# Kernel optimization log

Hardware: AMD Instinct MI355X
Metric: run time of the kernel (lower is better)

## Reference

```python
import jax, jax.numpy as jnp
import numpy as np

B = 4; E_PER = 100_000; E = B * E_PER
N_NODES = 50_000; N_REL = 500; D = 64; D_LG = 256
K_PER_VI = 20; S_VI = E // K_PER_VI          # 20000 sorted vi segments
S_VJ_PER = 5_000; S_VJ = B * S_VJ_PER        # 20000 unsorted vj segments
N_MEM = 131_072
INTERACT = ((0, 3), (0, 2, 3), (0, 4), (0, 2, 4), (1, 3), (1, 2, 3), (1, 4), (1, 2, 4))


def _build_edges():
    rng = np.random.default_rng(0)
    idx_vi = np.repeat(np.arange(S_VI), K_PER_VI)          # sorted segment ids
    gpb = S_VI // B
    eg = idx_vi // gpb                                     # sorted by eg_idx too
    vi = rng.integers(0, N_NODES, S_VI)[idx_vi]
    idx_vj = np.empty(E, dtype=np.int64)
    for b in range(B):
        loc = np.concatenate([np.arange(S_VJ_PER), rng.integers(0, S_VJ_PER, E_PER - S_VJ_PER)])
        rng.shuffle(loc)
        idx_vj[b * E_PER:(b + 1) * E_PER] = b * S_VJ_PER + loc  # every group non-empty
    vj = rng.integers(0, N_NODES, S_VJ)[idx_vj]            # consistent (eg, vj) per group
    rel = rng.integers(0, N_REL, E)
    e2vi = rng.integers(0, N_MEM, E)
    e2vj = rng.integers(0, N_MEM, E)
    return np.stack([eg, vi, vj, rel, idx_vi, idx_vj, e2vi, e2vj], axis=1).astype(np.int32)


def setup_inputs() -> dict:
    key = jax.random.key(0)
    ks = jax.random.split(key, 10)
    return {
        "node_attention": jax.random.uniform(ks[0], (B, N_NODES), jnp.float32),
        "scanned_edges": jnp.asarray(_build_edges()),
        "edges_y": jax.random.uniform(ks[1], (E,), jnp.float32),
        "hidden_uncon": jax.random.normal(ks[2], (1, N_NODES, D_LG), jnp.float32),
        "hidden_con": jax.random.normal(ks[3], (N_MEM, D), jnp.float32),
        "Wc": jax.random.normal(ks[4], (D, D), jnp.float32) / np.sqrt(D).astype(np.float32),
        "bc": jnp.zeros((D,), jnp.float32),
        "Wu": jax.random.normal(ks[5], (D_LG, D), jnp.float32) / np.sqrt(D_LG).astype(np.float32),
        "bu": jnp.zeros((D,), jnp.float32),
        "rel_table": jax.random.normal(ks[6], (N_REL, D), jnp.float32) * 0.05,
        "ws": jax.random.normal(ks[7], (len(INTERACT), D), jnp.float32) / np.sqrt(float(len(INTERACT))).astype(np.float32) if False else jax.random.normal(ks[7], (len(INTERACT), D), jnp.float32) * (1.0 / np.sqrt(len(INTERACT)).astype(np.float32)),
        "fb": jnp.zeros((D,), jnp.float32),
        "out_w": jax.random.normal(ks[8], (D,), jnp.float32),
        "out_b": jnp.zeros((D,), jnp.float32),
        "n_vi_segments": S_VI,
        "n_vj_segments": S_VJ,
    }


def reference(node_attention, scanned_edges, edges_y, hidden_uncon, hidden_con,
              Wc, bc, Wu, bu, rel_table, ws, fb, out_w, out_b,
              n_vi_segments, n_vj_segments):
    eg, vi, vj, rel = (scanned_edges[:, i] for i in range(4))
    idx_vi, idx_vj, e2vi, e2vj = (scanned_edges[:, i] for i in range(4, 8))
    # projections (proj_con / proj_uncon, tanh Dense)
    hc = jnp.tanh(hidden_con @ Wc + bc)          # [N_MEM, D]
    hu = jnp.tanh(hidden_uncon @ Wu + bu)[0]     # [n_nodes, D]; batch_size==1 path of Node2Edge
    # Node2Edge gathers
    feats = (hc[e2vi], hu[vi], rel_table[rel], hc[e2vj], hu[vj])  # each [E, D]
    # F layer: weighted sum of elementwise interaction products
    out = fb
    for k, idxs in enumerate(INTERACT):
        x = feats[idxs[0]]
        for i in idxs[1:]:
            x = x * feats[i]
        out = out + x * ws[k]
    out = jax.nn.relu(out) * out_w + out_b
    logits = jnp.sum(out, axis=1)                # [E]
    # NeighborSoftmax at 'vi' (sorted segment softmax)
    m = jax.ops.segment_max(logits, idx_vi, num_segments=n_vi_segments)
    ex = jnp.exp(logits - m[idx_vi])
    den = jax.ops.segment_sum(ex, idx_vi, num_segments=n_vi_segments)
    transition = ex / den[idx_vi]
    # attention flow: gather source attention, weight, aggregate at vj
    trans_att = transition * node_attention[eg, vi] * edges_y
    aggr = jax.ops.segment_sum(trans_att, idx_vj, num_segments=n_vj_segments)
    b_g = jax.ops.segment_max(eg, idx_vj, num_segments=n_vj_segments)
    vj_g = jax.ops.segment_max(vj, idx_vj, num_segments=n_vj_segments)
    new_node_attention = jnp.zeros_like(node_attention).at[b_g, vj_g].add(aggr)
    return new_node_attention
```

## Files before the change

kernel.cpp:

```cpp
#include <hip/hip_runtime.h>
#include <hip/hip_bf16.h>
#include <type_traits>

#define D 64
#define KPER 20

typedef __attribute__((ext_vector_type(8))) short short8;
typedef __attribute__((ext_vector_type(4))) float floatx4;

__device__ __forceinline__ unsigned short f2bfu(float x) {
    __hip_bfloat16 h = __float2bfloat16(x);
    return *reinterpret_cast<unsigned short*>(&h);
}
__device__ __forceinline__ float bfu2f(unsigned short u) {
    return __uint_as_float(((unsigned)u) << 16);
}

__device__ __forceinline__ float fast_tanh(float x) {
    float xc = fminf(fmaxf(x, -15.f), 15.f);
    float e = __expf(2.f * xc);
    return 1.f - 2.f * __builtin_amdgcn_rcpf(1.f + e);
}

template<int CTRL>
__device__ __forceinline__ float dpp_add(float x) {
    int t = __builtin_amdgcn_update_dpp(0, __float_as_int(x), CTRL, 0xf, 0xf, true);
    return x + __int_as_float(t);
}
template<int CTRL>
__device__ __forceinline__ float dpp_max(float x) {
    int xi = __float_as_int(x);
    int t = __builtin_amdgcn_update_dpp(xi, xi, CTRL, 0xf, 0xf, false);
    return fmaxf(x, __int_as_float(t));
}
__device__ __forceinline__ float wave_sum_b(float x) {
    x = dpp_add<0x111>(x); x = dpp_add<0x112>(x);
    x = dpp_add<0x114>(x); x = dpp_add<0x118>(x);
    x = dpp_add<0x142>(x); x = dpp_add<0x143>(x);
    return __int_as_float(__builtin_amdgcn_readlane(__float_as_int(x), 63));
}
__device__ __forceinline__ float wave_max_b(float x) {
    x = dpp_max<0x111>(x); x = dpp_max<0x112>(x);
    x = dpp_max<0x114>(x); x = dpp_max<0x118>(x);
    x = dpp_max<0x142>(x); x = dpp_max<0x143>(x);
    return __int_as_float(__builtin_amdgcn_readlane(__float_as_int(x), 63));
}
__device__ __forceinline__ float row16_sum(float x) {
    x = dpp_add<0x111>(x); x = dpp_add<0x112>(x);
    x = dpp_add<0x114>(x); x = dpp_add<0x118>(x);
    return x;
}

__global__ __launch_bounds__(256) void prep(
        const float* __restrict__ Wc, const float* __restrict__ Wu,
        const float* __restrict__ relf,
        unsigned short* __restrict__ Wcp, unsigned short* __restrict__ Wup,
        unsigned short* __restrict__ relb, float* __restrict__ outz,
        int nout, int nrel) {
    int tid = blockIdx.x * 256 + threadIdx.x;
    int nth = gridDim.x * 256;
    for (int i = tid; i < 4 * 2 * 64 * 8; i += nth) {
        int j = i & 7, lane = (i >> 3) & 63, f = i >> 9;
        int ct = f >> 1, kt = f & 1;
        int m = lane & 15, quad = lane >> 4;
        Wcp[i] = f2bfu(Wc[(kt * 32 + quad * 8 + j) * 64 + ct * 16 + m]);
    }
    for (int i = tid; i < 4 * 8 * 64 * 8; i += nth) {
        int j = i & 7, lane = (i >> 3) & 63, f = i >> 9;
        int ct = f >> 3, kt = f & 7;
        int m = lane & 15, quad = lane >> 4;
        Wup[i] = f2bfu(Wu[(kt * 32 + quad * 8 + j) * 64 + ct * 16 + m]);
    }
    for (int i = tid; i < nrel; i += nth) relb[i] = f2bfu(relf[i]);
    for (int i = tid; i < nout; i += nth) outz[i] = 0.0f;
}

__device__ __forceinline__ void proj64_pair(const float* __restrict__ h,
        const unsigned short* __restrict__ Wp, const float* __restrict__ b,
        unsigned short* __restrict__ out, int rt0) {
    constexpr int K = 64, KT = 2, CTN = 4;
    int lane = threadIdx.x & 63;
    int m = lane & 15, quad = lane >> 4;
    short8 bfr[CTN][KT];
    #pragma unroll
    for (int ct = 0; ct < CTN; ++ct)
        #pragma unroll
        for (int kt = 0; kt < KT; ++kt)
            bfr[ct][kt] = *(const short8*)(Wp + (((ct * 2 + kt) * 64 + lane) << 3));
    float bv[CTN];
    #pragma unroll
    for (int ct = 0; ct < CTN; ++ct) bv[ct] = b[ct * 16 + m];
    int rt1 = rt0 + 1;
    const float* hrow0 = h + (size_t)(rt0 * 16 + m) * K + quad * 8;
    const float* hrow1 = h + (size_t)(rt1 * 16 + m) * K + quad * 8;
    floatx4 a0[KT][2], a1[KT][2];
    #pragma unroll
    for (int kt = 0; kt < KT; ++kt) {
        a0[kt][0] = *(const floatx4*)(hrow0 + kt * 32);
        a0[kt][1] = *(const floatx4*)(hrow0 + kt * 32 + 4);
        a1[kt][0] = *(const floatx4*)(hrow1 + kt * 32);
        a1[kt][1] = *(const floatx4*)(hrow1 + kt * 32 + 4);
    }
    #pragma unroll
    for (int t = 0; t < 2; ++t) {
        floatx4 (*ar)[2] = t ? a1 : a0;
        int rt = t ? rt1 : rt0;
        floatx4 acc[CTN];
        #pragma unroll
        for (int ct = 0; ct < CTN; ++ct) acc[ct] = floatx4{0.f, 0.f, 0.f, 0.f};
        #pragma unroll
        for (int kt = 0; kt < KT; ++kt) {
            short8 af;
            #pragma unroll
            for (int j = 0; j < 4; ++j) {
                af[j]     = (short)f2bfu(ar[kt][0][j]);
                af[j + 4] = (short)f2bfu(ar[kt][1][j]);
            }
            #pragma unroll
            for (int ct = 0; ct < CTN; ++ct)
                acc[ct] = __builtin_amdgcn_mfma_f32_16x16x32_bf16(af, bfr[ct][kt], acc[ct], 0, 0, 0);
        }
        #pragma unroll
        for (int ct = 0; ct < CTN; ++ct) {
            int col = ct * 16 + m;
            #pragma unroll
            for (int reg = 0; reg < 4; ++reg) {
                int row = rt * 16 + quad * 4 + reg;
                out[(size_t)row * 64 + col] = f2bfu(fast_tanh(acc[ct][reg] + bv[ct]));
            }
        }
    }
}

__device__ __forceinline__ void proj256_body(const float* __restrict__ h,
        const unsigned short* __restrict__ Wp, const float* __restrict__ b,
        unsigned short* __restrict__ out, int ct0, int rt0, int rtstride, int ntiles) {
    constexpr int K = 256, KT = 8, CTN = 2;
    int lane = threadIdx.x & 63;
    int m = lane & 15, quad = lane >> 4;
    short8 bfr[CTN][KT];
    #pragma unroll
    for (int ct = 0; ct < CTN; ++ct)
        #pragma unroll
        for (int kt = 0; kt < KT; ++kt)
            bfr[ct][kt] = *(const short8*)(Wp + ((((ct0 + ct) * 8 + kt) * 64 + lane) << 3));
    float bv[CTN];
    #pragma unroll
    for (int ct = 0; ct < CTN; ++ct) bv[ct] = b[(ct0 + ct) * 16 + m];
    for (int rt = rt0; rt < ntiles; rt += rtstride) {
        floatx4 acc[CTN];
        #pragma unroll
        for (int ct = 0; ct < CTN; ++ct) acc[ct] = floatx4{0.f, 0.f, 0.f, 0.f};
        const float* hrow = h + (size_t)(rt * 16 + m) * K + quad * 8;
        #pragma unroll
        for (int kt = 0; kt < KT; ++kt) {
            floatx4 v0 = *(const floatx4*)(hrow + kt * 32);
            floatx4 v1 = *(const floatx4*)(hrow + kt * 32 + 4);
            short8 af;
            #pragma unroll
            for (int j = 0; j < 4; ++j) {
                af[j]     = (short)f2bfu(v0[j]);
                af[j + 4] = (short)f2bfu(v1[j]);
            }
            #pragma unroll
            for (int ct = 0; ct < CTN; ++ct)
                acc[ct] = __builtin_amdgcn_mfma_f32_16x16x32_bf16(af, bfr[ct][kt], acc[ct], 0, 0, 0);
        }
        #pragma unroll
        for (int ct = 0; ct < CTN; ++ct) {
            int col = (ct0 + ct) * 16 + m;
            #pragma unroll
            for (int reg = 0; reg < 4; ++reg) {
                int row = rt * 16 + quad * 4 + reg;
                out[(size_t)row * 64 + col] = f2bfu(fast_tanh(acc[ct][reg] + bv[ct]));
            }
        }
    }
}

__global__ __launch_bounds__(256) void proj_fused(
        const float* __restrict__ hcon, const unsigned short* __restrict__ Wcp,
        const float* __restrict__ bc,
        const float* __restrict__ hun, const unsigned short* __restrict__ Wup,
        const float* __restrict__ bu,
        unsigned short* __restrict__ hc, unsigned short* __restrict__ hu,
        int t64, int t256, int g64, int g256) {
    int bid = blockIdx.x;
    int w = threadIdx.x >> 6;
    if (bid < g256) {
        int wid = bid * 4 + w;
        int half = wid & 1;
        proj256_body(hun, Wup, bu, hu, half * 2, wid >> 1, g256 * 2, t256);
    } else {
        int wid = (bid - g256) * 4 + w;
        proj64_pair(hcon, Wcp, bc, hc, wid * 2);
    }
}

__device__ __forceinline__ void unp4(uint2 u, float f[4]) {
    f[0] = __uint_as_float(u.x << 16);
    f[1] = __uint_as_float(u.x & 0xffff0000u);
    f[2] = __uint_as_float(u.y << 16);
    f[3] = __uint_as_float(u.y & 0xffff0000u);
}

__global__ __launch_bounds__(256) void edge_kernel(
        const float* __restrict__ natt, const int* __restrict__ edges,
        const float* __restrict__ ey, const unsigned short* __restrict__ hc,
        const unsigned short* __restrict__ hu, const unsigned short* __restrict__ relt,
        const float* __restrict__ wsm, const float* __restrict__ fb,
        const float* __restrict__ outw, float* __restrict__ out, int N) {
    int lane = threadIdx.x & 63;
    int g = lane >> 4, sub = lane & 15;
    int l2 = lane >> 2;
    int s = blockIdx.x * 4 + (threadIdx.x >> 6);
    long base = (long)s * KPER;
    const int* eb = edges + base * 8;
    int eg = __builtin_amdgcn_readfirstlane(eb[0]);
    int vi = __builtin_amdgcn_readfirstlane(eb[1]);

    const int* ebg = eb + g * 8;
    int vjx[5], relx[5], evix[5], evjx[5];
    #pragma unroll
    for (int i = 0; i < 5; ++i) {
        vjx[i]  = ebg[i * 32 + 2];
        relx[i] = ebg[i * 32 + 3];
        evix[i] = ebg[i * 32 + 6];
        evjx[i] = ebg[i * 32 + 7];
    }
    uint2 G0[5], G2[5], G3[5], G4[5];
    #pragma unroll
    for (int i = 0; i < 5; ++i) {
        G0[i] = *(const uint2*)(hc   + (size_t)evix[i] * D + sub * 4);
        G2[i] = *(const uint2*)(relt + (size_t)relx[i] * D + sub * 4);
        G3[i] = *(const uint2*)(hc   + (size_t)evjx[i] * D + sub * 4);
        G4[i] = *(const uint2*)(hu   + (size_t)vjx[i]  * D + sub * 4);
    }
    uint2 F1u = *(const uint2*)(hu + (size_t)vi * D + sub * 4);
    float f1[4];
    unp4(F1u, f1);

    floatx4 wv[8];
    #pragma unroll
    for (int k = 0; k < 8; ++k) wv[k] = *(const floatx4*)(wsm + k * D + sub * 4);
    floatx4 fbv = *(const floatx4*)(fb + sub * 4);
    floatx4 owv = *(const floatx4*)(outw + sub * 4);
    float na = natt[(size_t)eg * N + vi];

    float myl = -INFINITY;
    #pragma unroll
    for (int i = 0; i < 5; ++i) {
        float F0[4], F2[4], F3[4], F4[4];
        unp4(G0[i], F0); unp4(G2[i], F2); unp4(G3[i], F3); unp4(G4[i], F4);
        float acc = 0.f;
        #pragma unroll
        for (int j = 0; j < 4; ++j) {
            float t1 = fmaf(F2[j], wv[1][j], wv[0][j]);
            float t2 = fmaf(F2[j], wv[5][j], wv[4][j]);
            float t3 = fmaf(F2[j], wv[3][j], wv[2][j]);
            float t4 = fmaf(F2[j], wv[7][j], wv[6][j]);
            float u = fmaf(F0[j], t1, f1[j] * t2);
            float v = fmaf(F0[j], t3, f1[j] * t4);
            float od = fmaf(F3[j], u, fmaf(F4[j], v, fbv[j]));
            acc = fmaf(fmaxf(od, 0.f), owv[j], acc);
        }
        float rs = row16_sum(acc);
        float tot = __shfl(rs, ((lane & 3) << 4) + 15);
        myl = (l2 == i) ? tot : myl;
    }
    float mx = wave_max_b(myl);
    float ex = __expf(myl - mx);
    float den = wave_sum_b(ex);
    if (lane < KPER) {
        int myvj = eb[lane * 8 + 2];
        float t = (ex / den) * na * ey[base + lane];
        atomicAdd(out + (size_t)eg * N + myvj, t);
    }
}

extern "C" void kernel_launch(void* const* d_in, const int* in_sizes, int n_in,
                              void* d_out, int out_size, void* d_ws, size_t ws_size,
                              hipStream_t stream) {
    const float* natt = (const float*)d_in[0];
    const int*   edges = (const int*)d_in[1];
    const float* ey   = (const float*)d_in[2];
    const float* hun  = (const float*)d_in[3];
    const float* hcon = (const float*)d_in[4];
    const float* Wc   = (const float*)d_in[5];
    const float* bc   = (const float*)d_in[6];
    const float* Wu   = (const float*)d_in[7];
    const float* bu   = (const float*)d_in[8];
    const float* relt = (const float*)d_in[9];
    const float* wsm  = (const float*)d_in[10];
    const float* fb   = (const float*)d_in[11];
    const float* outw = (const float*)d_in[12];
    float* out = (float*)d_out;

    int E    = in_sizes[2];
    int S    = E / KPER;
    int nmem = in_sizes[4] / D;
    int N    = in_sizes[3] / 256;
    int nrel = in_sizes[9];

    int t64  = nmem / 16;
    int t256 = N / 16;
    int g64  = t64 / 8;
    int g256 = 800;

    unsigned short* hc  = (unsigned short*)d_ws;
    unsigned short* hu  = hc + (size_t)nmem * D;
    unsigned short* rb  = hu + (size_t)N * D;
    unsigned short* Wcp = rb + nrel;
    unsigned short* Wup = Wcp + 4096;

    prep<<<64, 256, 0, stream>>>(Wc, Wu, relt, Wcp, Wup, rb, out, out_size, nrel);
    proj_fused<<<g256 + g64, 256, 0, stream>>>(hcon, Wcp, bc, hun, Wup, bu,
                                               hc, hu, t64, t256, g64, g256);
    edge_kernel<<<S / 4, 256, 0, stream>>>(natt, edges, ey, hc, hu, rb,
                                           wsm, fb, outw, out, N);
}
```

Baseline: 202.7 us.

## Switch edge features to packed fp16 math and process two segments per wave

Projected features, relation table, interaction weights and bias are now stored as fp16 instead of bf16, so the edge interaction products can run as packed half2 FMAs. Each wave now handles two vi segments, with gathers for both issued before compute, which gives more memory-level parallelism and halves the grid. Edge index loads are merged into int2 reads. The trade-offs are fp16 range/precision risk on the products and higher register pressure from holding two segments' gathers.

```diff
diff --git a/kernel.cpp b/kernel.cpp
--- a/kernel.cpp
+++ b/kernel.cpp
@@ -1,6 +1,6 @@
 #include <hip/hip_runtime.h>
 #include <hip/hip_bf16.h>
-#include <type_traits>
+#include <hip/hip_fp16.h>
 
 #define D 64
 #define KPER 20
@@ -12,8 +12,17 @@
     __hip_bfloat16 h = __float2bfloat16(x);
     return *reinterpret_cast<unsigned short*>(&h);
 }
-__device__ __forceinline__ float bfu2f(unsigned short u) {
-    return __uint_as_float(((unsigned)u) << 16);
+__device__ __forceinline__ unsigned short f2hu(float x) {
+    __half h = __float2half(x);
+    return *reinterpret_cast<unsigned short*>(&h);
+}
+union UH2 { unsigned u; __half2 h; };
+__device__ __forceinline__ __half2 u2h2(unsigned u) { UH2 x; x.u = u; return x.h; }
+
+__device__ __forceinline__ __half2 pk_max(__half2 a, __half2 b) {
+    __half2 r;
+    asm("v_pk_max_f16 %0, %1, %2" : "=v"(r) : "v"(a), "v"(b));
+    return r;
 }
 
 __device__ __forceinline__ float fast_tanh(float x) {
@@ -53,9 +62,11 @@
 
 __global__ __launch_bounds__(256) void prep(
         const float* __restrict__ Wc, const float* __restrict__ Wu,
-        const float* __restrict__ relf,
+        const float* __restrict__ relf, const float* __restrict__ wsf,
+        const float* __restrict__ fbf,
         unsigned short* __restrict__ Wcp, unsigned short* __restrict__ Wup,
-        unsigned short* __restrict__ relb, float* __restrict__ outz,
+        unsigned short* __restrict__ relb, unsigned short* __restrict__ wsh,
+        unsigned short* __restrict__ fbh, float* __restrict__ outz,
         int nout, int nrel) {
     int tid = blockIdx.x * 256 + threadIdx.x;
     int nth = gridDim.x * 256;
@@ -71,7 +82,9 @@
         int m = lane & 15, quad = lane >> 4;
         Wup[i] = f2bfu(Wu[(kt * 32 + quad * 8 + j) * 64 + ct * 16 + m]);
     }
-    for (int i = tid; i < nrel; i += nth) relb[i] = f2bfu(relf[i]);
+    for (int i = tid; i < nrel; i += nth) relb[i] = f2hu(relf[i]);
+    for (int i = tid; i < 8 * D; i += nth) wsh[i] = f2hu(wsf[i]);
+    for (int i = tid; i < D; i += nth) fbh[i] = f2hu(fbf[i]);
     for (int i = tid; i < nout; i += nth) outz[i] = 0.0f;
 }
 
@@ -126,7 +139,7 @@
             #pragma unroll
             for (int reg = 0; reg < 4; ++reg) {
                 int row = rt * 16 + quad * 4 + reg;
-                out[(size_t)row * 64 + col] = f2bfu(fast_tanh(acc[ct][reg] + bv[ct]));
+                out[(size_t)row * 64 + col] = f2hu(fast_tanh(acc[ct][reg] + bv[ct]));
             }
         }
     }
@@ -172,7 +185,7 @@
             #pragma unroll
             for (int reg = 0; reg < 4; ++reg) {
                 int row = rt * 16 + quad * 4 + reg;
-                out[(size_t)row * 64 + col] = f2bfu(fast_tanh(acc[ct][reg] + bv[ct]));
+                out[(size_t)row * 64 + col] = f2hu(fast_tanh(acc[ct][reg] + bv[ct]));
             }
         }
     }
@@ -197,84 +210,131 @@
     }
 }
 
-__device__ __forceinline__ void unp4(uint2 u, float f[4]) {
-    f[0] = __uint_as_float(u.x << 16);
-    f[1] = __uint_as_float(u.x & 0xffff0000u);
-    f[2] = __uint_as_float(u.y << 16);
-    f[3] = __uint_as_float(u.y & 0xffff0000u);
+__device__ __forceinline__ float seg_myl(
+        const uint2* __restrict__ G0, const uint2* __restrict__ G2,
+        const uint2* __restrict__ G3, const uint2* __restrict__ G4,
+        uint2 F1u, const uint2* __restrict__ wku, uint2 fbu, floatx4 owv,
+        int lane, int l2, __half2 z2) {
+    __half2 f1[2]  = { u2h2(F1u.x), u2h2(F1u.y) };
+    __half2 fb2[2] = { u2h2(fbu.x), u2h2(fbu.y) };
+    float myl = -INFINITY;
+    #pragma unroll
+    for (int i = 0; i < 5; ++i) {
+        float acc = 0.f;
+        #pragma unroll
+        for (int p = 0; p < 2; ++p) {
+            __half2 F0 = u2h2(p ? G0[i].y : G0[i].x);
+            __half2 F2 = u2h2(p ? G2[i].y : G2[i].x);
+            __half2 F3 = u2h2(p ? G3[i].y : G3[i].x);
+            __half2 F4 = u2h2(p ? G4[i].y : G4[i].x);
+            __half2 w0 = u2h2(p ? wku[0].y : wku[0].x);
+            __half2 w1 = u2h2(p ? wku[1].y : wku[1].x);
+            __half2 w2 = u2h2(p ? wku[2].y : wku[2].x);
+            __half2 w3 = u2h2(p ? wku[3].y : wku[3].x);
+            __half2 w4 = u2h2(p ? wku[4].y : wku[4].x);
+            __half2 w5 = u2h2(p ? wku[5].y : wku[5].x);
+            __half2 w6 = u2h2(p ? wku[6].y : wku[6].x);
+            __half2 w7 = u2h2(p ? wku[7].y : wku[7].x);
+            __half2 t1 = __hfma2(F2, w1, w0);
+            __half2 t2 = __hfma2(F2, w5, w4);
+            __half2 t3 = __hfma2(F2, w3, w2);
+            __half2 t4 = __hfma2(F2, w7, w6);
+            __half2 uu = __hfma2(F0, t1, __hmul2(f1[p], t2));
+            __half2 vv = __hfma2(F0, t3, __hmul2(f1[p], t4));
+            __half2 od = __hfma2(F3, uu, __hfma2(F4, vv, fb2[p]));
+            __half2 r  = pk_max(od, z2);
+            float2 rf  = __half22float2(r);
+            acc = fmaf(rf.x, owv[2 * p], fmaf(rf.y, owv[2 * p + 1], acc));
+        }
+        float rs = row16_sum(acc);
+        float tot = __shfl(rs, ((lane & 3) << 4) + 15);
+        myl = (l2 == i) ? tot : myl;
+    }
+    return myl;
 }
 
 __global__ __launch_bounds__(256) void edge_kernel(
         const float* __restrict__ natt, const int* __restrict__ edges,
         const float* __restrict__ ey, const unsigned short* __restrict__ hc,
         const unsigned short* __restrict__ hu, const unsigned short* __restrict__ relt,
-        const float* __restrict__ wsm, const float* __restrict__ fb,
+        const unsigned short* __restrict__ wsh, const unsigned short* __restrict__ fbh,
         const float* __restrict__ outw, float* __restrict__ out, int N) {
     int lane = threadIdx.x & 63;
     int g = lane >> 4, sub = lane & 15;
     int l2 = lane >> 2;
-    int s = blockIdx.x * 4 + (threadIdx.x >> 6);
-    long base = (long)s * KPER;
-    const int* eb = edges + base * 8;
-    int eg = __builtin_amdgcn_readfirstlane(eb[0]);
-    int vi = __builtin_amdgcn_readfirstlane(eb[1]);
-
-    const int* ebg = eb + g * 8;
-    int vjx[5], relx[5], evix[5], evjx[5];
+    int wid = blockIdx.x * 4 + (threadIdx.x >> 6);
+    long baseA = (long)(wid * 2) * KPER;
+    long baseB = baseA + KPER;
+    const int* ebA = edges + baseA * 8;
+    const int* ebB = edges + baseB * 8;
+
+    int2 h0A = *(const int2*)ebA;
+    int2 h0B = *(const int2*)ebB;
+    const int* egpA = ebA + g * 8;
+    const int* egpB = ebB + g * 8;
+    int2 m23A[5], m67A[5], m23B[5], m67B[5];
     #pragma unroll
     for (int i = 0; i < 5; ++i) {
-        vjx[i]  = ebg[i * 32 + 2];
-        relx[i] = ebg[i * 32 + 3];
-        evix[i] = ebg[i * 32 + 6];
-        evjx[i] = ebg[i * 32 + 7];
-    }
-    uint2 G0[5], G2[5], G3[5], G4[5];
+        m23A[i] = *(const int2*)(egpA + i * 32 + 2);
+        m67A[i] = *(const int2*)(egpA + i * 32 + 6);
+        m23B[i] = *(const int2*)(egpB + i * 32 + 2);
+        m67B[i] = *(const int2*)(egpB + i * 32 + 6);
+    }
+    int myvjA = 0, myvjB = 0; float eyA = 0.f, eyB = 0.f;
+    if (lane < KPER) {
+        myvjA = ebA[lane * 8 + 2];
+        myvjB = ebB[lane * 8 + 2];
+        eyA = ey[baseA + lane];
+        eyB = ey[baseB + lane];
+    }
+    int egA = __builtin_amdgcn_readfirstlane(h0A.x);
+    int viA = __builtin_amdgcn_readfirstlane(h0A.y);
+    int egB = __builtin_amdgcn_readfirstlane(h0B.x);
+    int viB = __builtin_amdgcn_readfirstlane(h0B.y);
+
+    uint2 GA0[5], GA2[5], GA3[5], GA4[5];
     #pragma unroll
     for (int i = 0; i < 5; ++i) {
-        G0[i] = *(const uint2*)(hc   + (size_t)evix[i] * D + sub * 4);
-        G2[i] = *(const uint2*)(relt + (size_t)relx[i] * D + sub * 4);
-        G3[i] = *(const uint2*)(hc   + (size_t)evjx[i] * D + sub * 4);
-        G4[i] = *(const uint2*)(hu   + (size_t)vjx[i]  * D + sub * 4);
-    }
-    uint2 F1u = *(const uint2*)(hu + (size_t)vi * D + sub * 4);
-    float f1[4];
-    unp4(F1u, f1);
-
-    floatx4 wv[8];
-    #pragma unroll
-    for (int k = 0; k < 8; ++k) wv[k] = *(const floatx4*)(wsm + k * D + sub * 4);
-    floatx4 fbv = *(const floatx4*)(fb + sub * 4);
+        GA0[i] = *(const uint2*)(hc   + (size_t)m67A[i].x * D + sub * 4);
+        GA2[i] = *(const uint2*)(relt + (size_t)m23A[i].y * D + sub * 4);
+        GA3[i] = *(const uint2*)(hc   + (size_t)m67A[i].y * D + sub * 4);
+        GA4[i] = *(const uint2*)(hu   + (size_t)m23A[i].x * D + sub * 4);
+    }
+    uint2 F1A = *(const uint2*)(hu + (size_t)viA * D + sub * 4);
+    uint2 GB0[5], GB2[5], GB3[5], GB4[5];
+    #pragma unroll
+    for (int i = 0; i < 5; ++i) {
+        GB0[i] = *(const uint2*)(hc   + (size_t)m67B[i].x * D + sub * 4);
+        GB2[i] = *(const uint2*)(relt + (size_t)m23B[i].y * D + sub * 4);
+        GB3[i] = *(const uint2*)(hc   + (size_t)m67B[i].y * D + sub * 4);
+        GB4[i] = *(const uint2*)(hu   + (size_t)m23B[i].x * D + sub * 4);
+    }
+    uint2 F1B = *(const uint2*)(hu + (size_t)viB * D + sub * 4);
+    float naA = natt[(size_t)egA * N + viA];
+    float naB = natt[(size_t)egB * N + viB];
+
+    uint2 wku[8];
+    #pragma unroll
+    for (int k = 0; k < 8; ++k) wku[k] = *(const uint2*)(wsh + k * D + sub * 4);
+    uint2 fbu = *(const uint2*)(fbh + sub * 4);
     floatx4 owv = *(const floatx4*)(outw + sub * 4);
-    float na = natt[(size_t)eg * N + vi];
-
-    float myl = -INFINITY;
-    #pragma unroll
-    for (int i = 0; i < 5; ++i) {
-        float F0[4], F2[4], F3[4], F4[4];
-        unp4(G0[i], F0); unp4(G2[i], F2); unp4(G3[i], F3); unp4(G4[i], F4);
-        float acc = 0.f;
-        #pragma unroll
-        for (int j = 0; j < 4; ++j) {
-            float t1 = fmaf(F2[j], wv[1][j], wv[0][j]);
-            float t2 = fmaf(F2[j], wv[5][j], wv[4][j]);
-            float t3 = fmaf(F2[j], wv[3][j], wv[2][j]);
-            float t4 = fmaf(F2[j], wv[7][j], wv[6][j]);
-            float u = fmaf(F0[j], t1, f1[j] * t2);
-            float v = fmaf(F0[j], t3, f1[j] * t4);
-            float od = fmaf(F3[j], u, fmaf(F4[j], v, fbv[j]));
-            acc = fmaf(fmaxf(od, 0.f), owv[j], acc);
-        }
-        float rs = row16_sum(acc);
-        float tot = __shfl(rs, ((lane & 3) << 4) + 15);
-        myl = (l2 == i) ? tot : myl;
-    }
-    float mx = wave_max_b(myl);
-    float ex = __expf(myl - mx);
-    float den = wave_sum_b(ex);
+    __half2 z2 = __float2half2_rn(0.f);
+
+    float mylA = seg_myl(GA0, GA2, GA3, GA4, F1A, wku, fbu, owv, lane, l2, z2);
+    float mxA = wave_max_b(mylA);
+    float exA = __expf(mylA - mxA);
+    float denA = wave_sum_b(exA);
     if (lane < KPER) {
-        int myvj = eb[lane * 8 + 2];
-        float t = (ex / den) * na * ey[base + lane];
-        atomicAdd(out + (size_t)eg * N + myvj, t);
+        float t = (exA / denA) * naA * eyA;
+        atomicAdd(out + (size_t)egA * N + myvjA, t);
+    }
+    float mylB = seg_myl(GB0, GB2, GB3, GB4, F1B, wku, fbu, owv, lane, l2, z2);
+    float mxB = wave_max_b(mylB);
+    float exB = __expf(mylB - mxB);
+    float denB = wave_sum_b(exB);
+    if (lane < KPER) {
+        float t = (exB / denB) * naB * eyB;
+        atomicAdd(out + (size_t)egB * N + myvjB, t);
     }
 }
 
@@ -312,10 +372,13 @@
     unsigned short* rb  = hu + (size_t)N * D;
     unsigned short* Wcp = rb + nrel;
     unsigned short* Wup = Wcp + 4096;
-
-    prep<<<64, 256, 0, stream>>>(Wc, Wu, relt, Wcp, Wup, rb, out, out_size, nrel);
+    unsigned short* wsh = Wup + 16384;
+    unsigned short* fbh = wsh + 8 * D;
+
+    prep<<<64, 256, 0, stream>>>(Wc, Wu, relt, wsm, fb, Wcp, Wup, rb, wsh, fbh,
+                                 out, out_size, nrel);
     proj_fused<<<g256 + g64, 256, 0, stream>>>(hcon, Wcp, bc, hun, Wup, bu,
                                                hc, hu, t64, t256, g64, g256);
-    edge_kernel<<<S / 4, 256, 0, stream>>>(natt, edges, ey, hc, hu, rb,
-                                           wsm, fb, outw, out, N);
-}
+    edge_kernel<<<S / 8, 256, 0, stream>>>(natt, edges, ey, hc, hu, rb,
+                                           wsh, fbh, outw, out, N);
+}
```

New measurement: 198.1 us. -2.3%, faster.
